# Kernel optimization log

Hardware: AMD Instinct MI355X
Metric: run time of the kernel (lower is better)

Reference implementation:

```python
import jax, jax.numpy as jnp
import numpy as np

B_, T_, D_MODEL = 2, 1024, 1024
D_STATE, D_CONV, EXPAND = 16, 4, 2
D_INNER = D_MODEL * EXPAND


def setup_inputs() -> dict:
    key = jax.random.key(0)
    ks = jax.random.split(key, 12)
    def s(k, shape, sc=0.02):
        return jax.random.normal(k, shape, jnp.float32) * sc
    return {
        "x": jax.random.normal(ks[0], (B_, T_, D_MODEL), jnp.float32),
        "ln_g": jnp.ones((D_MODEL,), jnp.float32),
        "ln_b": jnp.zeros((D_MODEL,), jnp.float32),
        "W_in": s(ks[1], (D_MODEL, 2 * D_INNER)),
        "b_in": s(ks[2], (2 * D_INNER,)),
        "conv_w": s(ks[3], (D_INNER, 1, D_CONV)),  # depthwise kernel, torch OIH layout
        "conv_b": s(ks[4], (D_INNER,)),
        "A": s(ks[5], (D_INNER, D_STATE), 0.1),
        "W_B": s(ks[6], (D_INNER, D_STATE)),
        "b_B": s(ks[7], (D_STATE,)),
        "W_C": s(ks[8], (D_INNER, D_STATE)),
        "b_C": s(ks[9], (D_STATE,)),
        "D": jnp.ones((D_INNER,), jnp.float32),
        "W_out": s(ks[10], (D_INNER, D_MODEL)),
        "b_out": s(ks[11], (D_MODEL,)),
    }


def _ssm_forward(x, ln_g, ln_b, W_in, b_in, conv_w, conv_b, A, W_B, b_B, W_C, b_C, D, W_out, b_out):
    eps = 1e-5
    # LayerNorm (biased variance, as in torch)
    mu = jnp.mean(x, axis=-1, keepdims=True)
    var = jnp.var(x, axis=-1, keepdims=True)
    xn = (x - mu) / jnp.sqrt(var + eps) * ln_g + ln_b
    # in_proj -> split into x path and gate
    proj = xn @ W_in + b_in                      # (b, t, 2*d_inner)
    xp, gate = jnp.split(proj, 2, axis=-1)
    # depthwise causal conv1d (padding=d_conv-1 on the left == torch pad + truncate)
    xc = jax.lax.conv_general_dilated(
        xp.transpose(0, 2, 1), conv_w,
        window_strides=(1,), padding=[(D_CONV - 1, 0)],
        dimension_numbers=("NCH", "OIH", "NCH"),
        feature_group_count=D_INNER,
    ).transpose(0, 2, 1) + conv_b                # (b, t, d_inner)
    xc = jax.nn.silu(xc)
    Bt = xc @ W_B + b_B                          # (b, t, d_state)
    Ct = xc @ W_C + b_C                          # (b, t, d_state)
    a = jax.nn.sigmoid(A)                        # (d_inner, d_state), per-channel decay
    u = Bt[:, :, None, :] * xc[:, :, :, None]    # (b, t, d_inner, d_state)
    a_full = jnp.broadcast_to(a, u.shape)
    # h_t = a * h_{t-1} + u_t  via first-order-recurrence associative scan
    def combine(c1, c2):
        a1, u1 = c1
        a2, u2 = c2
        return a2 * a1, a2 * u1 + u2
    _, h = jax.lax.associative_scan(combine, (a_full, u), axis=1)
    y = jnp.einsum("btns,bts->btn", h, Ct) + D * xc
    y = y * jax.nn.silu(gate)
    return y @ W_out + b_out + x                 # residual (dropout is identity in eval)


def reference(x, ln_g, ln_b, W_in, b_in, conv_w, conv_b, A, W_B, b_B, W_C, b_C, D, W_out, b_out):
    return _ssm_forward(x, ln_g, ln_b, W_in, b_in, conv_w, conv_b, A, W_B, b_B, W_C, b_C, D, W_out, b_out)
```

## Files before the change

kernel.cpp:

```cpp
#include <hip/hip_runtime.h>
#include <hip/hip_bf16.h>
#include <stdint.h>

using u16 = unsigned short;
typedef short bf16x8 __attribute__((ext_vector_type(8)));
typedef float f32x4 __attribute__((ext_vector_type(4)));

__device__ __forceinline__ float b2f(u16 u) {
  union { unsigned int i; float f; } v; v.i = ((unsigned int)u) << 16; return v.f;
}
__device__ __forceinline__ u16 f2b(float f) {
  __hip_bfloat16 h = __float2bfloat16(f);
  u16 r; __builtin_memcpy(&r, &h, 2); return r;
}
__device__ __forceinline__ bool probe_bf16(const void* p) {
  return *(const unsigned int*)p == 0x3F803F80u;
}
__device__ __forceinline__ float loadf(const void* p, size_t i, bool bf) {
  return bf ? b2f(((const u16*)p)[i]) : ((const float*)p)[i];
}
__device__ __forceinline__ void gload_lds16(const u16* g, u16* l) {
  __builtin_amdgcn_global_load_lds(
      (const __attribute__((address_space(1))) unsigned int*)(g),
      (__attribute__((address_space(3))) unsigned int*)(l),
      16, 0, 0);
}
template <int BK>
__device__ __forceinline__ int swkey(int row) {
  if constexpr (BK == 32) return (row >> 1) & 3;
  else return row & (BK / 8 - 1);
}

__global__ void transpose_any_k(const void* __restrict__ in, u16* __restrict__ out,
                                int R, int C, const void* __restrict__ probe) {
  const bool bf = probe_bf16(probe);
  __shared__ u16 tile[32][33];
  int c0 = blockIdx.x * 32, r0 = blockIdx.y * 32;
  int tx = threadIdx.x, ty = threadIdx.y;
#pragma unroll
  for (int i = 0; i < 4; i++) {
    size_t idx = (size_t)(r0 + ty + i * 8) * C + c0 + tx;
    tile[ty + i * 8][tx] = bf ? ((const u16*)in)[idx] : f2b(((const float*)in)[idx]);
  }
  __syncthreads();
#pragma unroll
  for (int i = 0; i < 4; i++)
    out[(size_t)(c0 + ty + i * 8) * R + r0 + tx] = tile[tx][ty + i * 8];
}

__launch_bounds__(256)
__global__ void ln_kernel(const void* __restrict__ x, const void* __restrict__ g,
                          const void* __restrict__ b, u16* __restrict__ xn) {
  const bool bf = probe_bf16(g);
  const int row = blockIdx.x, tid = threadIdx.x;
  const size_t base = (size_t)row * 1024;
  float v[4]; float s = 0.f, s2 = 0.f;
#pragma unroll
  for (int i = 0; i < 4; i++) {
    v[i] = loadf(x, base + tid + i * 256, bf);
    s += v[i]; s2 += v[i] * v[i];
  }
#pragma unroll
  for (int m = 32; m >= 1; m >>= 1) { s += __shfl_xor(s, m); s2 += __shfl_xor(s2, m); }
  __shared__ float rs[4], rs2[4];
  if ((tid & 63) == 0) { rs[tid >> 6] = s; rs2[tid >> 6] = s2; }
  __syncthreads();
  s = rs[0] + rs[1] + rs[2] + rs[3];
  s2 = rs2[0] + rs2[1] + rs2[2] + rs2[3];
  float mu = s * (1.f / 1024.f);
  float var = s2 * (1.f / 1024.f) - mu * mu;
  float rstd = rsqrtf(var + 1e-5f);
#pragma unroll
  for (int i = 0; i < 4; i++) {
    int c = tid + i * 256;
    float o = (v[i] - mu) * rstd * loadf(g, c, bf) + loadf(b, c, bf);
    xn[base + c] = f2b(o);
  }
}

template <int ROWS, int BK>
__device__ __forceinline__ void stage_tile(const u16* __restrict__ g, u16* lbuf,
                                           int K, int wave, int lane) {
  constexpr int LPR = BK / 8;
  constexpr int RPI = 512 / BK;
  constexpr int NI = ROWS / RPI;
  const int lr = lane / LPR, lc = lane % LPR;
#pragma unroll
  for (int j = wave; j < NI; j += 4) {
    int row = j * RPI + lr;
    int col = (lc ^ swkey<BK>(row)) * 8;
    gload_lds16(g + (size_t)row * K + col, lbuf + (size_t)j * RPI * BK);
  }
}

template <int BM, int BN, int BK, bool RESID, bool DUALOUT, bool PARTIAL>
__launch_bounds__(256)
__global__ void gemm_async(const u16* __restrict__ A, const u16* __restrict__ BT,
                           const void* __restrict__ bias, const void* __restrict__ resid,
                           void* __restrict__ Cout, float* __restrict__ Cpart,
                           int M, int N, int K, int k_len,
                           const void* __restrict__ probe) {
  constexpr int WM = BM / 2, WN = BN / 2;
  constexpr int TM = WM / 16, TN = WN / 16;
  constexpr int KF = BK / 32;
  __shared__ __align__(16) u16 lds[2][(BM + BN) * BK];
  const int tid = threadIdx.x;
  const int bm = blockIdx.x, bn = blockIdx.y, bz = blockIdx.z;
  const int lane = tid & 63, wave = tid >> 6;
  const int wm = wave >> 1, wn = wave & 1;
  const int lrow = lane & 15, quad = lane >> 4;
  f32x4 acc[TM][TN] = {};
  const u16* Ag = A + (size_t)bm * BM * K + (size_t)bz * k_len;
  const u16* Bg = BT + (size_t)bn * BN * K + (size_t)bz * k_len;

  stage_tile<BM, BK>(Ag, &lds[0][0], K, wave, lane);
  stage_tile<BN, BK>(Bg, &lds[0][BM * BK], K, wave, lane);
  __syncthreads();

  int cur = 0;
  for (int k0 = 0; k0 < k_len; k0 += BK, cur ^= 1) {
    if (k0 + BK < k_len) {
      stage_tile<BM, BK>(Ag + k0 + BK, &lds[cur ^ 1][0], K, wave, lane);
      stage_tile<BN, BK>(Bg + k0 + BK, &lds[cur ^ 1][BM * BK], K, wave, lane);
    }
    const u16* bufA = &lds[cur][0];
    const u16* bufB = &lds[cur][BM * BK];
#pragma unroll
    for (int f = 0; f < KF; f++) {
      bf16x8 af[TM], bv[TN];
#pragma unroll
      for (int i = 0; i < TM; i++) {
        int row = wm * WM + i * 16 + lrow;
        af[i] = *(const bf16x8*)&bufA[(size_t)row * BK + (((f * 4 + quad) ^ swkey<BK>(row)) * 8)];
      }
#pragma unroll
      for (int j = 0; j < TN; j++) {
        int row = wn * WN + j * 16 + lrow;
        bv[j] = *(const bf16x8*)&bufB[(size_t)row * BK + (((f * 4 + quad) ^ swkey<BK>(row)) * 8)];
      }
#pragma unroll
      for (int i = 0; i < TM; i++)
#pragma unroll
        for (int j = 0; j < TN; j++)
          acc[i][j] = __builtin_amdgcn_mfma_f32_16x16x32_bf16(af[i], bv[j], acc[i][j], 0, 0, 0);
    }
    __syncthreads();
  }

  if constexpr (PARTIAL) {
    float* P = Cpart + (size_t)bz * M * N;
#pragma unroll
    for (int i = 0; i < TM; i++)
#pragma unroll
      for (int j = 0; j < TN; j++) {
        int col = bn * BN + wn * WN + j * 16 + lrow;
#pragma unroll
        for (int r = 0; r < 4; r++) {
          int row = bm * BM + wm * WM + i * 16 + quad * 4 + r;
          P[(size_t)row * N + col] = acc[i][j][r];
        }
      }
    return;
  }

  const bool bf = probe_bf16(probe);
#pragma unroll
  for (int i = 0; i < TM; i++) {
#pragma unroll
    for (int j = 0; j < TN; j++) {
      int col = bn * BN + wn * WN + j * 16 + lrow;
      float bvv = loadf(bias, col, bf);
#pragma unroll
      for (int r = 0; r < 4; r++) {
        int row = bm * BM + wm * WM + i * 16 + quad * 4 + r;
        float v = acc[i][j][r] + bvv;
        if constexpr (RESID) v += loadf(resid, (size_t)row * N + col, bf);
        if constexpr (DUALOUT) {
          if (bf) ((u16*)Cout)[(size_t)row * N + col] = f2b(v);
          else    ((float*)Cout)[(size_t)row * N + col] = v;
        } else {
          ((u16*)Cout)[(size_t)row * N + col] = f2b(v);
        }
      }
    }
  }
}

__launch_bounds__(256)
__global__ void reduce_out(const float* __restrict__ p, const void* __restrict__ bias,
                           const void* __restrict__ resid, void* __restrict__ out,
                           const void* __restrict__ probe) {
  const bool bf = probe_bf16(probe);
  const int row = blockIdx.x, c0 = threadIdx.x * 4;
  const size_t i = (size_t)row * 1024 + c0;
  f32x4 a = *(const f32x4*)(p + i);
  f32x4 b = *(const f32x4*)(p + (size_t)2048 * 1024 + i);
  float o[4];
#pragma unroll
  for (int e = 0; e < 4; e++)
    o[e] = a[e] + b[e] + loadf(bias, c0 + e, bf) + loadf(resid, i + e, bf);
  if (bf) {
    u16 pk[4];
#pragma unroll
    for (int e = 0; e < 4; e++) pk[e] = f2b(o[e]);
    *(uint2*)((u16*)out + i) = *(uint2*)pk;
  } else {
    f32x4 v; v[0] = o[0]; v[1] = o[1]; v[2] = o[2]; v[3] = o[3];
    *(f32x4*)((float*)out + i) = v;
  }
}

__launch_bounds__(256)
__global__ void conv_bc_kernel(const u16* __restrict__ proj, const void* __restrict__ cw,
                               const void* __restrict__ cb, const void* __restrict__ WB,
                               const void* __restrict__ bB, const void* __restrict__ WC,
                               const void* __restrict__ bC, u16* __restrict__ xcb,
                               float* __restrict__ BC, const void* __restrict__ probe) {
  const bool bf = probe_bf16(probe);
  __shared__ float xr[2112];
  __shared__ float red[8][33];
  const int row = blockIdx.x, tid = threadIdx.x;
  const int t = row & 1023;
  const int n0 = tid * 8;
  float acc[8];
#pragma unroll
  for (int e = 0; e < 8; e++) acc[e] = loadf(cb, n0 + e, bf);
#pragma unroll
  for (int k = 0; k < 4; k++) {
    if (t - 3 + k >= 0) {
      union { int4 v; u16 u[8]; } uu;
      uu.v = *(const int4*)(proj + (size_t)(row - 3 + k) * 4096 + n0);
#pragma unroll
      for (int e = 0; e < 8; e++)
        acc[e] = __builtin_fmaf(b2f(uu.u[e]), loadf(cw, (n0 + e) * 4 + k, bf), acc[e]);
    }
  }
  {
    union { int4 v; u16 u[8]; } pk;
    int base = n0 + (n0 >> 5);
#pragma unroll
    for (int e = 0; e < 8; e++) {
      float s = acc[e];
      float xv = s / (1.f + __expf(-s));
      xr[base + e] = xv;
      pk.u[e] = f2b(xv);
    }
    *(int4*)(xcb + (size_t)row * 2048 + n0) = pk.v;
  }
  __syncthreads();
  const int c = tid & 31, sl = tid >> 5, cc = c & 15;
  const void* W = (c < 16) ? WB : WC;
  float p = 0.f;
  int k = sl * 256;
  if (bf) {
    const u16* W16 = (const u16*)W;
#pragma unroll 8
    for (int kk = 0; kk < 256; kk++, k++)
      p = __builtin_fmaf(xr[k + (k >> 5)], b2f(W16[k * 16 + cc]), p);
  } else {
    const float* W32 = (const float*)W;
#pragma unroll 8
    for (int kk = 0; kk < 256; kk++, k++)
      p = __builtin_fmaf(xr[k + (k >> 5)], W32[k * 16 + cc], p);
  }
  red[sl][c] = p;
  __syncthreads();
  if (tid < 32) {
    float s = 0.f;
#pragma unroll
    for (int i = 0; i < 8; i++) s += red[i][tid];
    s += (tid < 16) ? loadf(bB, tid, bf) : loadf(bC, tid - 16, bf);
    BC[(size_t)row * 32 + tid] = s;
  }
}


__launch_bounds__(256)
__global__ void scan_pass1(const u16* __restrict__ xc, const float* __restrict__ BC,
                           const void* __restrict__ Abuf, float* __restrict__ carry,
                           const void* __restrict__ probe) {
  const bool bf = probe_bf16(probe);
  const int tid = threadIdx.x;
  const int c = blockIdx.x & 15, ng = (blockIdx.x >> 4) & 7, bi = blockIdx.x >> 7;
  const int n = ng * 256 + tid;
  float a[16], h[16];
#pragma unroll
  for (int s = 0; s < 16; s++) {
    float av = loadf(Abuf, n * 16 + s, bf);
    a[s] = 1.f / (1.f + __expf(-av));
    h[s] = 0.f;
  }
  __shared__ __align__(16) u16 xs[32 * 256];
  __shared__ __align__(16) float bcs[32 * 32];
  const u16* xcp = xc + (size_t)bi * 1024 * 2048 + ng * 256;
  const float* bcp = BC + (size_t)bi * 1024 * 32;
  for (int half = 0; half < 2; half++) {
    const int tc = c * 64 + half * 32;
    __syncthreads();
#pragma unroll
    for (int i = 0; i < 4; i++) {
      int ch = tid + i * 256;
      int r = ch >> 5, cv = (ch & 31) * 8;
      *(int4*)&xs[ch * 8] = *(const int4*)(xcp + (size_t)(tc + r) * 2048 + cv);
    }
    {
      int r = tid >> 3, cv = (tid & 7) * 4;
      *(int4*)&bcs[tid * 4] = *(const int4*)(bcp + (size_t)(tc + r) * 32 + cv);
    }
    __syncthreads();
    for (int t = 0; t < 32; t++) {
      float x = b2f(xs[t * 256 + tid]);
#pragma unroll
      for (int s = 0; s < 16; s++)
        h[s] = __builtin_fmaf(a[s], h[s], bcs[t * 32 + s] * x);
    }
  }
  float* cp = carry + ((size_t)(bi * 16 + c) * 2048 + n) * 16;
#pragma unroll
  for (int s = 0; s < 16; s++) cp[s] = h[s];
}

__launch_bounds__(256)
__global__ void scan_prefix(float* __restrict__ carry, const void* __restrict__ Abuf,
                            const void* __restrict__ probe) {
  const bool bf = probe_bf16(probe);
  const int g = blockIdx.x * 256 + threadIdx.x;
  const int s = g & 15, n = (g >> 4) & 2047, bi = g >> 15;
  float a = 1.f / (1.f + __expf(-loadf(Abuf, n * 16 + s, bf)));
  float aL = a;
#pragma unroll
  for (int i = 0; i < 6; i++) aL = aL * aL;
  float running = 0.f;
  for (int c = 0; c < 16; c++) {
    size_t idx = ((size_t)(bi * 16 + c) * 2048 + n) * 16 + s;
    float tmp = carry[idx];
    carry[idx] = running;
    running = __builtin_fmaf(aL, running, tmp);
  }
}

__launch_bounds__(256)
__global__ void scan_pass2(const u16* __restrict__ xc, const u16* __restrict__ proj,
                           const float* __restrict__ BC, const void* __restrict__ Abuf,
                           const void* __restrict__ Dbuf, const float* __restrict__ carry,
                           u16* __restrict__ ybar, const void* __restrict__ probe) {
  const bool bf = probe_bf16(probe);
  const int tid = threadIdx.x;
  const int c = blockIdx.x & 15, ng = (blockIdx.x >> 4) & 7, bi = blockIdx.x >> 7;
  const int n = ng * 256 + tid;
  float a[16], h[16];
  const float* cp = carry + ((size_t)(bi * 16 + c) * 2048 + n) * 16;
#pragma unroll
  for (int s = 0; s < 16; s++) {
    float av = loadf(Abuf, n * 16 + s, bf);
    a[s] = 1.f / (1.f + __expf(-av));
    h[s] = cp[s];
  }
  const float Dn = loadf(Dbuf, n, bf);
  __shared__ __align__(16) u16 xs[32 * 256];
  __shared__ __align__(16) u16 gs[32 * 256];
  __shared__ __align__(16) float bcs[32 * 32];
  const u16* xcp = xc + (size_t)bi * 1024 * 2048 + ng * 256;
  const u16* gp = proj + (size_t)bi * 1024 * 4096 + 2048 + ng * 256;
  const float* bcp = BC + (size_t)bi * 1024 * 32;
  u16* yp = ybar + (size_t)bi * 1024 * 2048 + ng * 256;
  for (int half = 0; half < 2; half++) {
    const int tc = c * 64 + half * 32;
    __syncthreads();
#pragma unroll
    for (int i = 0; i < 4; i++) {
      int ch = tid + i * 256;
      int r = ch >> 5, cv = (ch & 31) * 8;
      *(int4*)&xs[ch * 8] = *(const int4*)(xcp + (size_t)(tc + r) * 2048 + cv);
      *(int4*)&gs[ch * 8] = *(const int4*)(gp + (size_t)(tc + r) * 4096 + cv);
    }
    {
      int r = tid >> 3, cv = (tid & 7) * 4;
      *(int4*)&bcs[tid * 4] = *(const int4*)(bcp + (size_t)(tc + r) * 32 + cv);
    }
    __syncthreads();
    for (int t = 0; t < 32; t++) {
      float x = b2f(xs[t * 256 + tid]);
      float acc = 0.f;
#pragma unroll
      for (int s = 0; s < 16; s++) {
        h[s] = __builtin_fmaf(a[s], h[s], bcs[t * 32 + s] * x);
        acc = __builtin_fmaf(h[s], bcs[t * 32 + 16 + s], acc);
      }
      float y = acc + Dn * x;
      float g = b2f(gs[t * 256 + tid]);
      float yg = y * g / (1.f + __expf(-g));
      yp[(size_t)(tc + t) * 2048 + tid] = f2b(yg);
    }
  }
}

extern "C" void kernel_launch(void* const* d_in, const int* in_sizes, int n_in,
                              void* d_out, int out_size, void* d_ws, size_t ws_size,
                              hipStream_t stream) {
  const void* x = d_in[0];
  const void* ln_g = d_in[1];
  const void* ln_b = d_in[2];
  const void* W_in = d_in[3];
  const void* b_in = d_in[4];
  const void* conv_w = d_in[5];
  const void* conv_b = d_in[6];
  const void* A = d_in[7];
  const void* W_B = d_in[8];
  const void* b_B = d_in[9];
  const void* W_C = d_in[10];
  const void* b_C = d_in[11];
  const void* Dp = d_in[12];
  const void* W_out = d_in[13];
  const void* b_out = d_in[14];
  const void* probe = ln_g;

  char* ws = (char*)d_ws;
  u16* WinT = (u16*)ws;
  u16* ybar = (u16*)ws;
  u16* xn = (u16*)(ws + (size_t)8 * 1024 * 1024);
  u16* WoutT = xn;
  u16* proj = (u16*)(ws + (size_t)12 * 1024 * 1024);
  u16* xcb = (u16*)(ws + (size_t)28 * 1024 * 1024);
  float* BC = (float*)(ws + (size_t)36 * 1024 * 1024);
  float* carry = (float*)(ws + (size_t)36 * 1024 * 1024 + 256 * 1024);
  float* part = (float*)(ws + (size_t)48 * 1024 * 1024);

  transpose_any_k<<<dim3(128, 32), dim3(32, 8), 0, stream>>>(W_in, WinT, 1024, 4096, probe);
  ln_kernel<<<2048, 256, 0, stream>>>(x, ln_g, ln_b, xn);
  gemm_async<128, 128, 64, false, false, false><<<dim3(16, 32), 256, 0, stream>>>(
      xn, WinT, b_in, nullptr, proj, nullptr, 2048, 4096, 1024, 1024, probe);
  transpose_any_k<<<dim3(32, 64), dim3(32, 8), 0, stream>>>(W_out, WoutT, 2048, 1024, probe);
  conv_bc_kernel<<<2048, 256, 0, stream>>>(proj, conv_w, conv_b, W_B, b_B, W_C, b_C,
                                           xcb, BC, probe);
  scan_pass1<<<256, 256, 0, stream>>>(xcb, BC, A, carry, probe);
  scan_prefix<<<256, 256, 0, stream>>>(carry, A, probe);
  scan_pass2<<<256, 256, 0, stream>>>(xcb, proj, BC, A, Dp, carry, ybar, probe);
  gemm_async<128, 64, 64, false, false, true><<<dim3(16, 16, 2), 256, 0, stream>>>(
      ybar, WoutT, nullptr, nullptr, nullptr, part, 2048, 1024, 2048, 1024, probe);
  reduce_out<<<2048, 256, 0, stream>>>(part, b_out, x, d_out, probe);
}
```

Baseline: 256.3 us.

## Split conv/SiLU from B/C projection and pre-pack B/C weights as bf16

```diff
diff --git a/kernel.cpp b/kernel.cpp
--- a/kernel.cpp
+++ b/kernel.cpp
@@ -46,6 +46,20 @@
 #pragma unroll
   for (int i = 0; i < 4; i++)
     out[(size_t)(c0 + ty + i * 8) * R + r0 + tx] = tile[tx][ty + i * 8];
+}
+
+__global__ void wbc_pack_k(const void* __restrict__ WB, const void* __restrict__ WC,
+                           u16* __restrict__ WT2, const void* __restrict__ probe) {
+  const bool bf = probe_bf16(probe);
+  const int g = blockIdx.x * 256 + threadIdx.x;
+  const int c = g & 31, kb = g >> 5;
+  const void* W = (c < 16) ? WB : WC;
+  const int cc = c & 15;
+  u16 pk[8];
+#pragma unroll
+  for (int e = 0; e < 8; e++) pk[e] = bf ? ((const u16*)W)[(kb * 8 + e) * 16 + cc]
+                                         : f2b(((const float*)W)[(kb * 8 + e) * 16 + cc]);
+  *(int4*)(WT2 + (size_t)g * 8) = *(int4*)pk;
 }
 
 __launch_bounds__(256)
@@ -210,58 +224,61 @@
   }
 }
 
-__launch_bounds__(256)
-__global__ void conv_bc_kernel(const u16* __restrict__ proj, const void* __restrict__ cw,
-                               const void* __restrict__ cb, const void* __restrict__ WB,
-                               const void* __restrict__ bB, const void* __restrict__ WC,
-                               const void* __restrict__ bC, u16* __restrict__ xcb,
-                               float* __restrict__ BC, const void* __restrict__ probe) {
-  const bool bf = probe_bf16(probe);
-  __shared__ float xr[2112];
+__global__ void conv_silu_kernel(const u16* __restrict__ proj, const void* __restrict__ cw,
+                                 const void* __restrict__ cb, u16* __restrict__ xc,
+                                 const void* __restrict__ probe) {
+  const bool bf = probe_bf16(probe);
+  const int n = blockIdx.x * 256 + threadIdx.x;
+  const int row = blockIdx.y;
+  const int t = row & 1023;
+  float w[4];
+#pragma unroll
+  for (int k = 0; k < 4; k++) w[k] = loadf(cw, n * 4 + k, bf);
+  float s = loadf(cb, n, bf);
+#pragma unroll
+  for (int k = 0; k < 4; k++) {
+    int tt = t - 3 + k;
+    if (tt >= 0) s += b2f(proj[(size_t)(row - 3 + k) * 4096 + n]) * w[k];
+  }
+  float sg = 1.f / (1.f + __expf(-s));
+  xc[(size_t)row * 2048 + n] = f2b(s * sg);
+}
+
+__launch_bounds__(256)
+__global__ void bc_proj2(const u16* __restrict__ xc, const u16* __restrict__ WT2,
+                         const void* __restrict__ bB, const void* __restrict__ bC,
+                         float* __restrict__ BC, const void* __restrict__ probe) {
+  const bool bf = probe_bf16(probe);
+  __shared__ __align__(16) float xr[2048];
   __shared__ float red[8][33];
   const int row = blockIdx.x, tid = threadIdx.x;
-  const int t = row & 1023;
-  const int n0 = tid * 8;
-  float acc[8];
-#pragma unroll
-  for (int e = 0; e < 8; e++) acc[e] = loadf(cb, n0 + e, bf);
-#pragma unroll
-  for (int k = 0; k < 4; k++) {
-    if (t - 3 + k >= 0) {
-      union { int4 v; u16 u[8]; } uu;
-      uu.v = *(const int4*)(proj + (size_t)(row - 3 + k) * 4096 + n0);
-#pragma unroll
-      for (int e = 0; e < 8; e++)
-        acc[e] = __builtin_fmaf(b2f(uu.u[e]), loadf(cw, (n0 + e) * 4 + k, bf), acc[e]);
-    }
-  }
+  const u16* xp = xc + (size_t)row * 2048;
   {
-    union { int4 v; u16 u[8]; } pk;
-    int base = n0 + (n0 >> 5);
-#pragma unroll
-    for (int e = 0; e < 8; e++) {
-      float s = acc[e];
-      float xv = s / (1.f + __expf(-s));
-      xr[base + e] = xv;
-      pk.u[e] = f2b(xv);
-    }
-    *(int4*)(xcb + (size_t)row * 2048 + n0) = pk.v;
+    int k0 = tid * 8;
+    union { int4 v; u16 u[8]; } uu;
+    uu.v = *(const int4*)(xp + k0);
+    f32x4 lo, hi;
+#pragma unroll
+    for (int e = 0; e < 4; e++) { lo[e] = b2f(uu.u[e]); hi[e] = b2f(uu.u[4 + e]); }
+    *(f32x4*)&xr[k0] = lo;
+    *(f32x4*)&xr[k0 + 4] = hi;
   }
   __syncthreads();
-  const int c = tid & 31, sl = tid >> 5, cc = c & 15;
-  const void* W = (c < 16) ? WB : WC;
+  const int c = tid & 31, sl = tid >> 5;
+  const float* xk = &xr[sl * 256];
   float p = 0.f;
-  int k = sl * 256;
-  if (bf) {
-    const u16* W16 = (const u16*)W;
-#pragma unroll 8
-    for (int kk = 0; kk < 256; kk++, k++)
-      p = __builtin_fmaf(xr[k + (k >> 5)], b2f(W16[k * 16 + cc]), p);
-  } else {
-    const float* W32 = (const float*)W;
-#pragma unroll 8
-    for (int kk = 0; kk < 256; kk++, k++)
-      p = __builtin_fmaf(xr[k + (k >> 5)], W32[k * 16 + cc], p);
+#pragma unroll 4
+  for (int j = 0; j < 32; j++) {
+    int kb = sl * 32 + j;
+    union { int4 v; u16 u[8]; } w8;
+    w8.v = *(const int4*)(WT2 + ((size_t)kb * 32 + c) * 8);
+    f32x4 x0 = *(const f32x4*)(xk + j * 8);
+    f32x4 x1 = *(const f32x4*)(xk + j * 8 + 4);
+#pragma unroll
+    for (int e = 0; e < 4; e++) {
+      p = __builtin_fmaf(x0[e], b2f(w8.u[e]), p);
+      p = __builtin_fmaf(x1[e], b2f(w8.u[4 + e]), p);
+    }
   }
   red[sl][c] = p;
   __syncthreads();
@@ -273,7 +290,6 @@
     BC[(size_t)row * 32 + tid] = s;
   }
 }
-
 
 __launch_bounds__(256)
 __global__ void scan_pass1(const u16* __restrict__ xc, const float* __restrict__ BC,
@@ -424,6 +440,7 @@
   u16* xcb = (u16*)(ws + (size_t)28 * 1024 * 1024);
   float* BC = (float*)(ws + (size_t)36 * 1024 * 1024);
   float* carry = (float*)(ws + (size_t)36 * 1024 * 1024 + 256 * 1024);
+  u16* WT2 = (u16*)(ws + (size_t)44 * 1024 * 1024);
   float* part = (float*)(ws + (size_t)48 * 1024 * 1024);
 
   transpose_any_k<<<dim3(128, 32), dim3(32, 8), 0, stream>>>(W_in, WinT, 1024, 4096, probe);
@@ -431,8 +448,9 @@
   gemm_async<128, 128, 64, false, false, false><<<dim3(16, 32), 256, 0, stream>>>(
       xn, WinT, b_in, nullptr, proj, nullptr, 2048, 4096, 1024, 1024, probe);
   transpose_any_k<<<dim3(32, 64), dim3(32, 8), 0, stream>>>(W_out, WoutT, 2048, 1024, probe);
-  conv_bc_kernel<<<2048, 256, 0, stream>>>(proj, conv_w, conv_b, W_B, b_B, W_C, b_C,
-                                           xcb, BC, probe);
+  wbc_pack_k<<<32, 256, 0, stream>>>(W_B, W_C, WT2, probe);
+  conv_silu_kernel<<<dim3(8, 2048), 256, 0, stream>>>(proj, conv_w, conv_b, xcb, probe);
+  bc_proj2<<<2048, 256, 0, stream>>>(xcb, WT2, b_B, b_C, BC, probe);
   scan_pass1<<<256, 256, 0, stream>>>(xcb, BC, A, carry, probe);
   scan_prefix<<<256, 256, 0, stream>>>(carry, A, probe);
   scan_pass2<<<256, 256, 0, stream>>>(xcb, proj, BC, A, Dp, carry, ybar, probe);
```

Result: faster. 227.5 us (-11.2%).
